# Optimization experiments

Measured on AMD Instinct MI355X. Metric: run time of the kernel, lower is better.

Reference implementation:

```python
import jax, jax.numpy as jnp
import numpy as np

B, S, H = 1, 1024, 1024
E = 1024          # expert_dim
NEXP = 16         # num_experts
TOPK = 2
ALPHA = 1.702
LIMIT = 7.0


def setup_inputs() -> dict:
    key = jax.random.key(0)
    ks = jax.random.split(key, 8)
    hidden_states = jax.random.normal(ks[0], (B, S, H), dtype=jnp.float32)
    # router (gate): Linear(H, NEXP) with bias
    Wg = jax.random.normal(ks[1], (NEXP, H), dtype=jnp.float32) / np.sqrt(H)
    bg = jax.random.normal(ks[2], (NEXP,), dtype=jnp.float32) * 0.01
    # per-expert gate_up_proj: Linear(H, 2E) -> store as [NEXP, H, 2E]
    Wgu = jax.random.normal(ks[3], (NEXP, H, 2 * E), dtype=jnp.float32) / np.sqrt(H)
    bgu = jax.random.normal(ks[4], (NEXP, 2 * E), dtype=jnp.float32) * 0.01
    # per-expert down_proj: Linear(E, H) -> store as [NEXP, E, H]
    Wd = jax.random.normal(ks[5], (NEXP, E, H), dtype=jnp.float32) / np.sqrt(E)
    bd = jax.random.normal(ks[6], (NEXP, H), dtype=jnp.float32) * 0.01
    return {"hidden_states": hidden_states, "Wg": Wg, "bg": bg,
            "Wgu": Wgu, "bgu": bgu, "Wd": Wd, "bd": bd}


def _moe_forward(x, Wg, bg, Wgu, bgu, Wd, bd):
    b, s, h = x.shape
    xt = x.reshape(-1, h)                                   # [T, H]
    # router
    logits = xt @ Wg.T + bg                                 # [T, NEXP]
    # gpt_oss routing: topk over raw logits, softmax over selected
    top_vals, top_idx = jax.lax.top_k(logits, TOPK)         # [T, K]
    rw = jax.nn.softmax(top_vals.astype(jnp.float32), axis=-1).astype(xt.dtype)
    # combine weight per (token, expert): zero for unselected experts
    onehot = jax.nn.one_hot(top_idx, NEXP, dtype=xt.dtype)  # [T, K, NEXP]
    cw = jnp.einsum("tk,tke->te", rw, onehot)               # [T, NEXP]
    # dense expert compute (reference math identical to gather/scatter version)
    gu = jnp.einsum("th,ehf->tef", xt, Wgu) + bgu[None]     # [T, NEXP, 2E]
    gate = gu[..., ::2]
    up = gu[..., 1::2]
    gate = jnp.minimum(gate, LIMIT)
    up = jnp.clip(up, -LIMIT, LIMIT)
    glu = gate * jax.nn.sigmoid(gate * ALPHA)
    gated = (up + 1.0) * glu                                # [T, NEXP, E]
    out_e = jnp.einsum("tef,efh->teh", gated, Wd) + bd[None]  # [T, NEXP, H]
    out = jnp.einsum("teh,te->th", out_e, cw)               # [T, H]
    return out.reshape(b, s, h)


def reference(hidden_states, Wg, bg, Wgu, bgu, Wd, bd):
    return _moe_forward(hidden_states, Wg, bg, Wgu, bgu, Wd, bd)
```

## Files before the change

### kernel.cpp

```cpp
#include <hip/hip_runtime.h>
#include <hip/hip_bf16.h>

#define NT 1024
#define HD 1024
#define ED 1024
#define F2D 2048
#define NEXPERT 16
#define GROWS 2304
#define ALPHA_C 1.702f
#define LIMIT_C 7.0f

typedef float f32x4 __attribute__((ext_vector_type(4)));
typedef short short8 __attribute__((ext_vector_type(8)));

__device__ __forceinline__ unsigned short f2bf(float x) {
  union { float f; unsigned int u; } v; v.f = x;
  unsigned int r = v.u + 0x7FFFu + ((v.u >> 16) & 1u);
  return (unsigned short)(r >> 16);
}
__device__ __forceinline__ unsigned int pk2(float lo, float hi) {
  return (unsigned int)f2bf(lo) | ((unsigned int)f2bf(hi) << 16);
}
__device__ __forceinline__ void async16(const void* g, void* l) {
  __builtin_amdgcn_global_load_lds((const __attribute__((address_space(1))) void*)g,
                                   (__attribute__((address_space(3))) void*)l, 16, 0, 0);
}

__global__ __launch_bounds__(64) void k_router(const float* __restrict__ x,
                                               const float* __restrict__ Wg,
                                               const float* __restrict__ bg,
                                               int* __restrict__ cnt,
                                               int* __restrict__ e01,
                                               float* __restrict__ w0f,
                                               float* __restrict__ w1f,
                                               unsigned short* __restrict__ Xbf) {
  const int t = blockIdx.x;
  const int l = threadIdx.x;
  const float4* x4 = (const float4*)(x + (size_t)t * HD);
  for (int i = 0; i < 4; ++i) {
    const int idx = l + 64 * i;
    float4 v = x4[idx];
    unsigned int a = pk2(v.x, v.y);
    unsigned int b = pk2(v.z, v.w);
    unsigned int* dst = (unsigned int*)(Xbf + (size_t)t * HD + idx * 4);
    dst[0] = a; dst[1] = b;
  }
  const int e = l & 15, qq = l >> 4;
  const float4* wg4 = (const float4*)(Wg + (size_t)e * HD);
  float s = 0.f;
  for (int j = 0; j < 64; ++j) {
    const int idx = qq + 4 * j;
    float4 a = x4[idx], b = wg4[idx];
    s += a.x * b.x + a.y * b.y + a.z * b.z + a.w * b.w;
  }
  s += __shfl_xor(s, 16);
  s += __shfl_xor(s, 32);
  const float logit = s + bg[e];
  float v0 = -1e30f, v1 = -1e30f; int i0 = 0, i1 = 0;
  for (int k = 0; k < 16; ++k) {
    float lv = __shfl(logit, k);
    if (lv > v0) { v1 = v0; i1 = i0; v0 = lv; i0 = k; }
    else if (lv > v1) { v1 = lv; i1 = k; }
  }
  if (l == 0) {
    float w0 = 1.f / (1.f + __expf(v1 - v0));
    atomicAdd(&cnt[i0], 1);
    atomicAdd(&cnt[i1], 1);
    e01[t] = i0 | (i1 << 8);
    w0f[t] = w0;
    w1f[t] = 1.f - w0;
  }
}

__global__ __launch_bounds__(1024) void k_scan_place(const int* __restrict__ cnt,
                                                     int* __restrict__ off,
                                                     const int* __restrict__ e01,
                                                     const float* __restrict__ w0f,
                                                     const float* __restrict__ w1f,
                                                     int* __restrict__ gtok,
                                                     float* __restrict__ gwt) {
  __shared__ int soff[NEXPERT];
  __shared__ int scur[NEXPERT];
  const int t = threadIdx.x;
  if (t == 0) {
    int a = 0;
    for (int e = 0; e < NEXPERT; ++e) { soff[e] = a; off[e] = a; a += cnt[e]; }
  }
  if (t < NEXPERT) scur[t] = 0;
  __syncthreads();
  const int p = e01[t];
  const int e0 = p & 255, e1 = p >> 8;
  int s0 = atomicAdd(&scur[e0], 1);
  int g0 = soff[e0] + s0;
  gtok[g0] = t; gwt[g0] = w0f[t];
  int s1 = atomicAdd(&scur[e1], 1);
  int g1 = soff[e1] + s1;
  gtok[g1] = t; gwt[g1] = w1f[t];
}

__global__ __launch_bounds__(256) void k_outinit(const float* __restrict__ bd,
                                                 const int* __restrict__ e01,
                                                 const float* __restrict__ w0f,
                                                 const float* __restrict__ w1f,
                                                 float* __restrict__ out) {
  const int t = blockIdx.x;
  const int h4 = threadIdx.x;
  const int p = e01[t];
  const int e0 = p & 255, e1 = p >> 8;
  const float w0 = w0f[t], w1 = w1f[t];
  float4 a = ((const float4*)(bd + (size_t)e0 * HD))[h4];
  float4 b = ((const float4*)(bd + (size_t)e1 * HD))[h4];
  float4 r;
  r.x = w0 * a.x + w1 * b.x;
  r.y = w0 * a.y + w1 * b.y;
  r.z = w0 * a.z + w1 * b.z;
  r.w = w0 * a.w + w1 * b.w;
  ((float4*)(out + (size_t)t * HD))[h4] = r;
}

__global__ __launch_bounds__(256) void k_gemm1(const unsigned short* __restrict__ Xbf,
                                               const float* __restrict__ Wgu,
                                               const float* __restrict__ bgu,
                                               const int* __restrict__ cnt,
                                               const int* __restrict__ off,
                                               const int* __restrict__ gtok,
                                               unsigned short* __restrict__ Gact) {
  const int e = blockIdx.z;
  const int Ne = cnt[e];
  const int mtile = blockIdx.y;
  if (mtile * 128 >= Ne) return;
  const int ntile = blockIdx.x;
  const int tid = threadIdx.x;
  const int lane = tid & 63;
  const int w = tid >> 6;
  const int wm = w & 1, wn = w >> 1;
  const int q = lane >> 4;
  const int fr = lane & 15;

  __shared__ unsigned short Alds[128 * 32];
  __shared__ unsigned int Blds[128 * 17];

  const int base = off[e] + mtile * 128;
  const int r0 = w * 32 + (lane >> 2);
  const int r1 = r0 + 16;
  const int c4 = lane & 3;
  const int gs0 = base + (((mtile * 128 + r0) < Ne) ? r0 : 0);
  const int gs1 = base + (((mtile * 128 + r1) < Ne) ? r1 : 0);
  const unsigned short* gp0 = Xbf + (size_t)gtok[gs0] * HD + c4 * 8;
  const unsigned short* gp1 = Xbf + (size_t)gtok[gs1] * HD + c4 * 8;
  unsigned short* la0 = Alds + w * 1024;
  unsigned short* la1 = Alds + w * 1024 + 512;
  const int k2 = tid >> 4;
  const int n8 = (tid & 15) * 8;
  const float* Wb = Wgu + (size_t)e * HD * F2D + (size_t)(2 * k2) * F2D + ntile * 128 + n8;

  f32x4 acc[4][4] = {};

  for (int ks = 0; ks < 32; ++ks) {
    __syncthreads();
    async16(gp0 + ks * 32, la0);
    async16(gp1 + ks * 32, la1);
    const float* bp = Wb + (size_t)ks * 32 * F2D;
    float4 a0 = *(const float4*)bp;
    float4 a1 = *(const float4*)(bp + 4);
    float4 b0 = *(const float4*)(bp + F2D);
    float4 b1 = *(const float4*)(bp + F2D + 4);
    Blds[(n8 + 0) * 17 + k2] = pk2(a0.x, b0.x);
    Blds[(n8 + 1) * 17 + k2] = pk2(a0.y, b0.y);
    Blds[(n8 + 2) * 17 + k2] = pk2(a0.z, b0.z);
    Blds[(n8 + 3) * 17 + k2] = pk2(a0.w, b0.w);
    Blds[(n8 + 4) * 17 + k2] = pk2(a1.x, b1.x);
    Blds[(n8 + 5) * 17 + k2] = pk2(a1.y, b1.y);
    Blds[(n8 + 6) * 17 + k2] = pk2(a1.z, b1.z);
    Blds[(n8 + 7) * 17 + k2] = pk2(a1.w, b1.w);
    __syncthreads();
    short8 af[4], bfr[4];
#pragma unroll
    for (int ni = 0; ni < 4; ++ni) {
      const unsigned int* p = Blds + (wn * 64 + ni * 16 + fr) * 17 + q * 4;
      union { unsigned int u[4]; short8 s; } uu;
      uu.u[0] = p[0]; uu.u[1] = p[1]; uu.u[2] = p[2]; uu.u[3] = p[3];
      bfr[ni] = uu.s;
    }
#pragma unroll
    for (int mi = 0; mi < 4; ++mi)
      af[mi] = *(const short8*)(Alds + (wm * 64 + mi * 16 + fr) * 32 + q * 8);
#pragma unroll
    for (int mi = 0; mi < 4; ++mi)
#pragma unroll
      for (int ni = 0; ni < 4; ++ni)
        acc[mi][ni] = __builtin_amdgcn_mfma_f32_16x16x32_bf16(af[mi], bfr[ni], acc[mi][ni], 0, 0, 0);
  }

  const float* bguE = bgu + (size_t)e * F2D + ntile * 128;
#pragma unroll
  for (int mi = 0; mi < 4; ++mi) {
    const int rowb = wm * 64 + mi * 16 + q * 4;
#pragma unroll
    for (int ni = 0; ni < 4; ++ni) {
      const int col = wn * 64 + ni * 16 + fr;
      const float bias = bguE[col];
#pragma unroll
      for (int r = 0; r < 4; ++r) {
        float v = acc[mi][ni][r] + bias;
        float pv = __shfl_xor(v, 1);
        float gate = (lane & 1) ? pv : v;
        float up   = (lane & 1) ? v : pv;
        gate = fminf(gate, LIMIT_C);
        up = fminf(fmaxf(up, -LIMIT_C), LIMIT_C);
        float glu = gate / (1.f + __expf(-ALPHA_C * gate));
        float val = (up + 1.f) * glu;
        const int s = rowb + r;
        if (!(lane & 1) && (mtile * 128 + s) < Ne)
          Gact[(size_t)(base + s) * ED + ntile * 64 + (col >> 1)] = f2bf(val);
      }
    }
  }
}

__global__ __launch_bounds__(256) void k_gemm2(const unsigned short* __restrict__ Gact,
                                               const float* __restrict__ Wd,
                                               const int* __restrict__ cnt,
                                               const int* __restrict__ off,
                                               const int* __restrict__ gtok,
                                               const float* __restrict__ gwt,
                                               float* __restrict__ out) {
  const int e = blockIdx.z;
  const int Ne = cnt[e];
  const int mtile = blockIdx.y;
  if (mtile * 128 >= Ne) return;
  const int ntile = blockIdx.x;
  const int tid = threadIdx.x;
  const int lane = tid & 63;
  const int w = tid >> 6;
  const int wm = w & 1, wn = w >> 1;
  const int q = lane >> 4;
  const int fr = lane & 15;

  __shared__ unsigned short Alds[128 * 32];
  __shared__ unsigned int Blds[128 * 17];

  const int base = off[e] + mtile * 128;
  const int r0 = w * 32 + (lane >> 2);
  const int r1 = r0 + 16;
  const int c4 = lane & 3;
  const unsigned short* gp0 = Gact + (size_t)(base + r0) * ED + c4 * 8;
  const unsigned short* gp1 = Gact + (size_t)(base + r1) * ED + c4 * 8;
  unsigned short* la0 = Alds + w * 1024;
  unsigned short* la1 = Alds + w * 1024 + 512;
  const int k2 = tid >> 4;
  const int n8 = (tid & 15) * 8;
  const float* Wb = Wd + (size_t)e * ED * HD + (size_t)(2 * k2) * HD + ntile * 128 + n8;

  f32x4 acc[4][4] = {};

  for (int ks = 0; ks < 32; ++ks) {
    __syncthreads();
    async16(gp0 + ks * 32, la0);
    async16(gp1 + ks * 32, la1);
    const float* bp = Wb + (size_t)ks * 32 * HD;
    float4 a0 = *(const float4*)bp;
    float4 a1 = *(const float4*)(bp + 4);
    float4 b0 = *(const float4*)(bp + HD);
    float4 b1 = *(const float4*)(bp + HD + 4);
    Blds[(n8 + 0) * 17 + k2] = pk2(a0.x, b0.x);
    Blds[(n8 + 1) * 17 + k2] = pk2(a0.y, b0.y);
    Blds[(n8 + 2) * 17 + k2] = pk2(a0.z, b0.z);
    Blds[(n8 + 3) * 17 + k2] = pk2(a0.w, b0.w);
    Blds[(n8 + 4) * 17 + k2] = pk2(a1.x, b1.x);
    Blds[(n8 + 5) * 17 + k2] = pk2(a1.y, b1.y);
    Blds[(n8 + 6) * 17 + k2] = pk2(a1.z, b1.z);
    Blds[(n8 + 7) * 17 + k2] = pk2(a1.w, b1.w);
    __syncthreads();
    short8 af[4], bfr[4];
#pragma unroll
    for (int ni = 0; ni < 4; ++ni) {
      const unsigned int* p = Blds + (wn * 64 + ni * 16 + fr) * 17 + q * 4;
      union { unsigned int u[4]; short8 s; } uu;
      uu.u[0] = p[0]; uu.u[1] = p[1]; uu.u[2] = p[2]; uu.u[3] = p[3];
      bfr[ni] = uu.s;
    }
#pragma unroll
    for (int mi = 0; mi < 4; ++mi)
      af[mi] = *(const short8*)(Alds + (wm * 64 + mi * 16 + fr) * 32 + q * 8);
#pragma unroll
    for (int mi = 0; mi < 4; ++mi)
#pragma unroll
      for (int ni = 0; ni < 4; ++ni)
        acc[mi][ni] = __builtin_amdgcn_mfma_f32_16x16x32_bf16(af[mi], bfr[ni], acc[mi][ni], 0, 0, 0);
  }

#pragma unroll
  for (int mi = 0; mi < 4; ++mi) {
    const int rowb = wm * 64 + mi * 16 + q * 4;
#pragma unroll
    for (int r = 0; r < 4; ++r) {
      const int s = rowb + r;
      if ((mtile * 128 + s) < Ne) {
        const int gsl = base + s;
        const int tok = gtok[gsl];
        const float wt = gwt[gsl];
        float* op = out + (size_t)tok * HD + ntile * 128;
#pragma unroll
        for (int ni = 0; ni < 4; ++ni) {
          const int col = wn * 64 + ni * 16 + fr;
          atomicAdd(op + col, wt * acc[mi][ni][r]);
        }
      }
    }
  }
}

extern "C" void kernel_launch(void* const* d_in, const int* in_sizes, int n_in,
                              void* d_out, int out_size, void* d_ws, size_t ws_size,
                              hipStream_t stream) {
  const float* x   = (const float*)d_in[0];
  const float* Wg  = (const float*)d_in[1];
  const float* bg  = (const float*)d_in[2];
  const float* Wgu = (const float*)d_in[3];
  const float* bgu = (const float*)d_in[4];
  const float* Wd  = (const float*)d_in[5];
  const float* bd  = (const float*)d_in[6];
  float* out = (float*)d_out;

  int* cnt = (int*)d_ws;
  int* off = cnt + 16;
  int* e01 = off + 16;
  float* w0f = (float*)(e01 + NT);
  float* w1f = w0f + NT;
  int* gtok = (int*)(w1f + NT);
  float* gwt = (float*)(gtok + GROWS);
  unsigned short* Xbf = (unsigned short*)(gwt + GROWS);
  unsigned short* Gact = Xbf + (size_t)NT * HD;

  hipMemsetAsync(cnt, 0, 16 * sizeof(int), stream);
  k_router<<<NT, 64, 0, stream>>>(x, Wg, bg, cnt, e01, w0f, w1f, Xbf);
  k_scan_place<<<1, NT, 0, stream>>>(cnt, off, e01, w0f, w1f, gtok, gwt);
  k_gemm1<<<dim3(16, 8, NEXPERT), 256, 0, stream>>>(Xbf, Wgu, bgu, cnt, off, gtok, Gact);
  k_outinit<<<NT, 256, 0, stream>>>(bd, e01, w0f, w1f, out);
  k_gemm2<<<dim3(8, 8, NEXPERT), 256, 0, stream>>>(Gact, Wd, cnt, off, gtok, gwt, out);
}
```

Measured before the change: 370.2 us.

## Double-buffer MoE GEMMs, shrink N tiles, split-K down proj, fuse routing kernels

Both expert GEMMs now double-buffer their LDS tiles. The next K-slice's weight loads and async activation copies are issued before the current slice's MFMAs, which removes one barrier per iteration. N tiles shrink from 128 to 64 columns and gemm2 adds a 2-way split-K, giving more blocks to fill the GPU on a memory-bound fp32 weight stream, plus a transposed B layout written with vector stores. The bias/output init moves into the router, and expert counting moves into the scan kernel, which drops a memset and a launch. The cost is more atomic adds to the output from split-K and smaller per-block reuse of the activation tiles.

```diff
diff --git a/kernel.cpp b/kernel.cpp
--- a/kernel.cpp
+++ b/kernel.cpp
@@ -12,6 +12,7 @@
 
 typedef float f32x4 __attribute__((ext_vector_type(4)));
 typedef short short8 __attribute__((ext_vector_type(8)));
+typedef unsigned int u32x4 __attribute__((ext_vector_type(4)));
 
 __device__ __forceinline__ unsigned short f2bf(float x) {
   union { float f; unsigned int u; } v; v.f = x;
@@ -29,11 +30,12 @@
 __global__ __launch_bounds__(64) void k_router(const float* __restrict__ x,
                                                const float* __restrict__ Wg,
                                                const float* __restrict__ bg,
-                                               int* __restrict__ cnt,
+                                               const float* __restrict__ bd,
                                                int* __restrict__ e01,
                                                float* __restrict__ w0f,
                                                float* __restrict__ w1f,
-                                               unsigned short* __restrict__ Xbf) {
+                                               unsigned short* __restrict__ Xbf,
+                                               float* __restrict__ out) {
   const int t = blockIdx.x;
   const int l = threadIdx.x;
   const float4* x4 = (const float4*)(x + (size_t)t * HD);
@@ -62,34 +64,51 @@
     if (lv > v0) { v1 = v0; i1 = i0; v0 = lv; i0 = k; }
     else if (lv > v1) { v1 = lv; i1 = k; }
   }
+  const float w0 = 1.f / (1.f + __expf(v1 - v0));
+  const float w1 = 1.f - w0;
   if (l == 0) {
-    float w0 = 1.f / (1.f + __expf(v1 - v0));
-    atomicAdd(&cnt[i0], 1);
-    atomicAdd(&cnt[i1], 1);
     e01[t] = i0 | (i1 << 8);
     w0f[t] = w0;
-    w1f[t] = 1.f - w0;
-  }
-}
-
-__global__ __launch_bounds__(1024) void k_scan_place(const int* __restrict__ cnt,
-                                                     int* __restrict__ off,
-                                                     const int* __restrict__ e01,
-                                                     const float* __restrict__ w0f,
-                                                     const float* __restrict__ w1f,
-                                                     int* __restrict__ gtok,
-                                                     float* __restrict__ gwt) {
+    w1f[t] = w1;
+  }
+  const float4* bd0 = (const float4*)(bd + (size_t)i0 * HD);
+  const float4* bd1 = (const float4*)(bd + (size_t)i1 * HD);
+  float4* o4 = (float4*)(out + (size_t)t * HD);
+  for (int i = 0; i < 4; ++i) {
+    const int idx = l + 64 * i;
+    float4 a = bd0[idx], b = bd1[idx];
+    float4 r;
+    r.x = w0 * a.x + w1 * b.x;
+    r.y = w0 * a.y + w1 * b.y;
+    r.z = w0 * a.z + w1 * b.z;
+    r.w = w0 * a.w + w1 * b.w;
+    o4[idx] = r;
+  }
+}
+
+__global__ __launch_bounds__(1024) void k_scan(const int* __restrict__ e01,
+                                               const float* __restrict__ w0f,
+                                               const float* __restrict__ w1f,
+                                               int* __restrict__ cnt,
+                                               int* __restrict__ off,
+                                               int* __restrict__ gtok,
+                                               float* __restrict__ gwt) {
+  __shared__ int scnt[NEXPERT];
   __shared__ int soff[NEXPERT];
   __shared__ int scur[NEXPERT];
   const int t = threadIdx.x;
+  if (t < NEXPERT) { scnt[t] = 0; scur[t] = 0; }
+  __syncthreads();
+  const int p = e01[t];
+  const int e0 = p & 255, e1 = p >> 8;
+  atomicAdd(&scnt[e0], 1);
+  atomicAdd(&scnt[e1], 1);
+  __syncthreads();
   if (t == 0) {
     int a = 0;
-    for (int e = 0; e < NEXPERT; ++e) { soff[e] = a; off[e] = a; a += cnt[e]; }
-  }
-  if (t < NEXPERT) scur[t] = 0;
-  __syncthreads();
-  const int p = e01[t];
-  const int e0 = p & 255, e1 = p >> 8;
+    for (int e = 0; e < NEXPERT; ++e) { soff[e] = a; off[e] = a; cnt[e] = scnt[e]; a += scnt[e]; }
+  }
+  __syncthreads();
   int s0 = atomicAdd(&scur[e0], 1);
   int g0 = soff[e0] + s0;
   gtok[g0] = t; gwt[g0] = w0f[t];
@@ -98,33 +117,13 @@
   gtok[g1] = t; gwt[g1] = w1f[t];
 }
 
-__global__ __launch_bounds__(256) void k_outinit(const float* __restrict__ bd,
-                                                 const int* __restrict__ e01,
-                                                 const float* __restrict__ w0f,
-                                                 const float* __restrict__ w1f,
-                                                 float* __restrict__ out) {
-  const int t = blockIdx.x;
-  const int h4 = threadIdx.x;
-  const int p = e01[t];
-  const int e0 = p & 255, e1 = p >> 8;
-  const float w0 = w0f[t], w1 = w1f[t];
-  float4 a = ((const float4*)(bd + (size_t)e0 * HD))[h4];
-  float4 b = ((const float4*)(bd + (size_t)e1 * HD))[h4];
-  float4 r;
-  r.x = w0 * a.x + w1 * b.x;
-  r.y = w0 * a.y + w1 * b.y;
-  r.z = w0 * a.z + w1 * b.z;
-  r.w = w0 * a.w + w1 * b.w;
-  ((float4*)(out + (size_t)t * HD))[h4] = r;
-}
-
-__global__ __launch_bounds__(256) void k_gemm1(const unsigned short* __restrict__ Xbf,
-                                               const float* __restrict__ Wgu,
-                                               const float* __restrict__ bgu,
-                                               const int* __restrict__ cnt,
-                                               const int* __restrict__ off,
-                                               const int* __restrict__ gtok,
-                                               unsigned short* __restrict__ Gact) {
+__global__ __launch_bounds__(256, 4) void k_gemm1(const unsigned short* __restrict__ Xbf,
+                                                  const float* __restrict__ Wgu,
+                                                  const float* __restrict__ bgu,
+                                                  const int* __restrict__ cnt,
+                                                  const int* __restrict__ off,
+                                                  const int* __restrict__ gtok,
+                                                  unsigned short* __restrict__ Gact) {
   const int e = blockIdx.z;
   const int Ne = cnt[e];
   const int mtile = blockIdx.y;
@@ -137,68 +136,81 @@
   const int q = lane >> 4;
   const int fr = lane & 15;
 
-  __shared__ unsigned short Alds[128 * 32];
-  __shared__ unsigned int Blds[128 * 17];
+  __shared__ unsigned short Alds[2 * 128 * 32];
+  __shared__ unsigned int Blds[2 * 16 * 68];
 
   const int base = off[e] + mtile * 128;
   const int r0 = w * 32 + (lane >> 2);
   const int r1 = r0 + 16;
-  const int c4 = lane & 3;
+  const int c4a = lane & 3;
   const int gs0 = base + (((mtile * 128 + r0) < Ne) ? r0 : 0);
   const int gs1 = base + (((mtile * 128 + r1) < Ne) ? r1 : 0);
-  const unsigned short* gp0 = Xbf + (size_t)gtok[gs0] * HD + c4 * 8;
-  const unsigned short* gp1 = Xbf + (size_t)gtok[gs1] * HD + c4 * 8;
-  unsigned short* la0 = Alds + w * 1024;
-  unsigned short* la1 = Alds + w * 1024 + 512;
+  const unsigned short* gp0 = Xbf + (size_t)gtok[gs0] * HD + c4a * 8;
+  const unsigned short* gp1 = Xbf + (size_t)gtok[gs1] * HD + c4a * 8;
+  const int lofs = w * 1024;
+
   const int k2 = tid >> 4;
-  const int n8 = (tid & 15) * 8;
-  const float* Wb = Wgu + (size_t)e * HD * F2D + (size_t)(2 * k2) * F2D + ntile * 128 + n8;
-
-  f32x4 acc[4][4] = {};
-
+  const int c4 = tid & 15;
+  const float* Wb = Wgu + (size_t)e * HD * F2D + (size_t)(2 * k2) * F2D + ntile * 64 + c4 * 4;
+
+  f32x4 acc[4][2] = {};
+  float4 ba, bb;
+
+  ba = *(const float4*)Wb;
+  bb = *(const float4*)(Wb + F2D);
+  async16(gp0, Alds + lofs);
+  async16(gp1, Alds + lofs + 512);
+  {
+    u32x4 pkv;
+    pkv[0] = pk2(ba.x, bb.x); pkv[1] = pk2(ba.y, bb.y);
+    pkv[2] = pk2(ba.z, bb.z); pkv[3] = pk2(ba.w, bb.w);
+    *(u32x4*)(Blds + k2 * 68 + c4 * 4) = pkv;
+  }
+  __syncthreads();
+
+#pragma unroll 2
   for (int ks = 0; ks < 32; ++ks) {
+    const int cur = ks & 1, nxt = cur ^ 1;
+    const bool more = (ks + 1) < 32;
+    if (more) {
+      const float* bp = Wb + (size_t)(ks + 1) * 32 * F2D;
+      ba = *(const float4*)bp;
+      bb = *(const float4*)(bp + F2D);
+      async16(gp0 + (ks + 1) * 32, Alds + nxt * 4096 + lofs);
+      async16(gp1 + (ks + 1) * 32, Alds + nxt * 4096 + lofs + 512);
+    }
+    short8 af[4], bfr[2];
+#pragma unroll
+    for (int mi = 0; mi < 4; ++mi)
+      af[mi] = *(const short8*)(Alds + cur * 4096 + (wm * 64 + mi * 16 + fr) * 32 + q * 8);
+#pragma unroll
+    for (int ni = 0; ni < 2; ++ni) {
+      const unsigned int* p = Blds + cur * 1088 + q * 4 * 68 + wn * 32 + ni * 16 + fr;
+      union { unsigned int u[4]; short8 s; } uu;
+      uu.u[0] = p[0]; uu.u[1] = p[68]; uu.u[2] = p[136]; uu.u[3] = p[204];
+      bfr[ni] = uu.s;
+    }
+#pragma unroll
+    for (int mi = 0; mi < 4; ++mi)
+#pragma unroll
+      for (int ni = 0; ni < 2; ++ni)
+        acc[mi][ni] = __builtin_amdgcn_mfma_f32_16x16x32_bf16(af[mi], bfr[ni], acc[mi][ni], 0, 0, 0);
+    if (more) {
+      u32x4 pkv;
+      pkv[0] = pk2(ba.x, bb.x); pkv[1] = pk2(ba.y, bb.y);
+      pkv[2] = pk2(ba.z, bb.z); pkv[3] = pk2(ba.w, bb.w);
+      *(u32x4*)(Blds + nxt * 1088 + k2 * 68 + c4 * 4) = pkv;
+    }
     __syncthreads();
-    async16(gp0 + ks * 32, la0);
-    async16(gp1 + ks * 32, la1);
-    const float* bp = Wb + (size_t)ks * 32 * F2D;
-    float4 a0 = *(const float4*)bp;
-    float4 a1 = *(const float4*)(bp + 4);
-    float4 b0 = *(const float4*)(bp + F2D);
-    float4 b1 = *(const float4*)(bp + F2D + 4);
-    Blds[(n8 + 0) * 17 + k2] = pk2(a0.x, b0.x);
-    Blds[(n8 + 1) * 17 + k2] = pk2(a0.y, b0.y);
-    Blds[(n8 + 2) * 17 + k2] = pk2(a0.z, b0.z);
-    Blds[(n8 + 3) * 17 + k2] = pk2(a0.w, b0.w);
-    Blds[(n8 + 4) * 17 + k2] = pk2(a1.x, b1.x);
-    Blds[(n8 + 5) * 17 + k2] = pk2(a1.y, b1.y);
-    Blds[(n8 + 6) * 17 + k2] = pk2(a1.z, b1.z);
-    Blds[(n8 + 7) * 17 + k2] = pk2(a1.w, b1.w);
-    __syncthreads();
-    short8 af[4], bfr[4];
-#pragma unroll
-    for (int ni = 0; ni < 4; ++ni) {
-      const unsigned int* p = Blds + (wn * 64 + ni * 16 + fr) * 17 + q * 4;
-      union { unsigned int u[4]; short8 s; } uu;
-      uu.u[0] = p[0]; uu.u[1] = p[1]; uu.u[2] = p[2]; uu.u[3] = p[3];
-      bfr[ni] = uu.s;
-    }
-#pragma unroll
-    for (int mi = 0; mi < 4; ++mi)
-      af[mi] = *(const short8*)(Alds + (wm * 64 + mi * 16 + fr) * 32 + q * 8);
-#pragma unroll
-    for (int mi = 0; mi < 4; ++mi)
-#pragma unroll
-      for (int ni = 0; ni < 4; ++ni)
-        acc[mi][ni] = __builtin_amdgcn_mfma_f32_16x16x32_bf16(af[mi], bfr[ni], acc[mi][ni], 0, 0, 0);
-  }
-
-  const float* bguE = bgu + (size_t)e * F2D + ntile * 128;
+  }
+
+  const float* bguE = bgu + (size_t)e * F2D + ntile * 64;
 #pragma unroll
   for (int mi = 0; mi < 4; ++mi) {
     const int rowb = wm * 64 + mi * 16 + q * 4;
 #pragma unroll
-    for (int ni = 0; ni < 4; ++ni) {
-      const int col = wn * 64 + ni * 16 + fr;
+    for (int ni = 0; ni < 2; ++ni) {
+      const int col = wn * 32 + ni * 16 + fr;
       const float bias = bguE[col];
 #pragma unroll
       for (int r = 0; r < 4; ++r) {
@@ -212,20 +224,21 @@
         float val = (up + 1.f) * glu;
         const int s = rowb + r;
         if (!(lane & 1) && (mtile * 128 + s) < Ne)
-          Gact[(size_t)(base + s) * ED + ntile * 64 + (col >> 1)] = f2bf(val);
+          Gact[(size_t)(base + s) * ED + ntile * 32 + (col >> 1)] = f2bf(val);
       }
     }
   }
 }
 
-__global__ __launch_bounds__(256) void k_gemm2(const unsigned short* __restrict__ Gact,
-                                               const float* __restrict__ Wd,
-                                               const int* __restrict__ cnt,
-                                               const int* __restrict__ off,
-                                               const int* __restrict__ gtok,
-                                               const float* __restrict__ gwt,
-                                               float* __restrict__ out) {
-  const int e = blockIdx.z;
+__global__ __launch_bounds__(256, 4) void k_gemm2(const unsigned short* __restrict__ Gact,
+                                                  const float* __restrict__ Wd,
+                                                  const int* __restrict__ cnt,
+                                                  const int* __restrict__ off,
+                                                  const int* __restrict__ gtok,
+                                                  const float* __restrict__ gwt,
+                                                  float* __restrict__ out) {
+  const int z = blockIdx.z;
+  const int e = z >> 1, ksp = z & 1;
   const int Ne = cnt[e];
   const int mtile = blockIdx.y;
   if (mtile * 128 >= Ne) return;
@@ -237,57 +250,70 @@
   const int q = lane >> 4;
   const int fr = lane & 15;
 
-  __shared__ unsigned short Alds[128 * 32];
-  __shared__ unsigned int Blds[128 * 17];
+  __shared__ unsigned short Alds[2 * 128 * 32];
+  __shared__ unsigned int Blds[2 * 16 * 68];
 
   const int base = off[e] + mtile * 128;
   const int r0 = w * 32 + (lane >> 2);
   const int r1 = r0 + 16;
-  const int c4 = lane & 3;
-  const unsigned short* gp0 = Gact + (size_t)(base + r0) * ED + c4 * 8;
-  const unsigned short* gp1 = Gact + (size_t)(base + r1) * ED + c4 * 8;
-  unsigned short* la0 = Alds + w * 1024;
-  unsigned short* la1 = Alds + w * 1024 + 512;
+  const int c4a = lane & 3;
+  const unsigned short* gp0 = Gact + (size_t)(base + r0) * ED + ksp * 512 + c4a * 8;
+  const unsigned short* gp1 = Gact + (size_t)(base + r1) * ED + ksp * 512 + c4a * 8;
+  const int lofs = w * 1024;
+
   const int k2 = tid >> 4;
-  const int n8 = (tid & 15) * 8;
-  const float* Wb = Wd + (size_t)e * ED * HD + (size_t)(2 * k2) * HD + ntile * 128 + n8;
-
-  f32x4 acc[4][4] = {};
-
-  for (int ks = 0; ks < 32; ++ks) {
+  const int c4 = tid & 15;
+  const float* Wb = Wd + (size_t)e * ED * HD + (size_t)(ksp * 512 + 2 * k2) * HD + ntile * 64 + c4 * 4;
+
+  f32x4 acc[4][2] = {};
+  float4 ba, bb;
+
+  ba = *(const float4*)Wb;
+  bb = *(const float4*)(Wb + HD);
+  async16(gp0, Alds + lofs);
+  async16(gp1, Alds + lofs + 512);
+  {
+    u32x4 pkv;
+    pkv[0] = pk2(ba.x, bb.x); pkv[1] = pk2(ba.y, bb.y);
+    pkv[2] = pk2(ba.z, bb.z); pkv[3] = pk2(ba.w, bb.w);
+    *(u32x4*)(Blds + k2 * 68 + c4 * 4) = pkv;
+  }
+  __syncthreads();
+
+#pragma unroll 2
+  for (int ks = 0; ks < 16; ++ks) {
+    const int cur = ks & 1, nxt = cur ^ 1;
+    const bool more = (ks + 1) < 16;
+    if (more) {
+      const float* bp = Wb + (size_t)(ks + 1) * 32 * HD;
+      ba = *(const float4*)bp;
+      bb = *(const float4*)(bp + HD);
+      async16(gp0 + (ks + 1) * 32, Alds + nxt * 4096 + lofs);
+      async16(gp1 + (ks + 1) * 32, Alds + nxt * 4096 + lofs + 512);
+    }
+    short8 af[4], bfr[2];
+#pragma unroll
+    for (int mi = 0; mi < 4; ++mi)
+      af[mi] = *(const short8*)(Alds + cur * 4096 + (wm * 64 + mi * 16 + fr) * 32 + q * 8);
+#pragma unroll
+    for (int ni = 0; ni < 2; ++ni) {
+      const unsigned int* p = Blds + cur * 1088 + q * 4 * 68 + wn * 32 + ni * 16 + fr;
+      union { unsigned int u[4]; short8 s; } uu;
+      uu.u[0] = p[0]; uu.u[1] = p[68]; uu.u[2] = p[136]; uu.u[3] = p[204];
+      bfr[ni] = uu.s;
+    }
+#pragma unroll
+    for (int mi = 0; mi < 4; ++mi)
+#pragma unroll
+      for (int ni = 0; ni < 2; ++ni)
+        acc[mi][ni] = __builtin_amdgcn_mfma_f32_16x16x32_bf16(af[mi], bfr[ni], acc[mi][ni], 0, 0, 0);
+    if (more) {
+      u32x4 pkv;
+      pkv[0] = pk2(ba.x, bb.x); pkv[1] = pk2(ba.y, bb.y);
+      pkv[2] = pk2(ba.z, bb.z); pkv[3] = pk2(ba.w, bb.w);
+      *(u32x4*)(Blds + nxt * 1088 + k2 * 68 + c4 * 4) = pkv;
+    }
     __syncthreads();
-    async16(gp0 + ks * 32, la0);
-    async16(gp1 + ks * 32, la1);
-    const float* bp = Wb + (size_t)ks * 32 * HD;
-    float4 a0 = *(const float4*)bp;
-    float4 a1 = *(const float4*)(bp + 4);
-    float4 b0 = *(const float4*)(bp + HD);
-    float4 b1 = *(const float4*)(bp + HD + 4);
-    Blds[(n8 + 0) * 17 + k2] = pk2(a0.x, b0.x);
-    Blds[(n8 + 1) * 17 + k2] = pk2(a0.y, b0.y);
-    Blds[(n8 + 2) * 17 + k2] = pk2(a0.z, b0.z);
-    Blds[(n8 + 3) * 17 + k2] = pk2(a0.w, b0.w);
-    Blds[(n8 + 4) * 17 + k2] = pk2(a1.x, b1.x);
-    Blds[(n8 + 5) * 17 + k2] = pk2(a1.y, b1.y);
-    Blds[(n8 + 6) * 17 + k2] = pk2(a1.z, b1.z);
-    Blds[(n8 + 7) * 17 + k2] = pk2(a1.w, b1.w);
-    __syncthreads();
-    short8 af[4], bfr[4];
-#pragma unroll
-    for (int ni = 0; ni < 4; ++ni) {
-      const unsigned int* p = Blds + (wn * 64 + ni * 16 + fr) * 17 + q * 4;
-      union { unsigned int u[4]; short8 s; } uu;
-      uu.u[0] = p[0]; uu.u[1] = p[1]; uu.u[2] = p[2]; uu.u[3] = p[3];
-      bfr[ni] = uu.s;
-    }
-#pragma unroll
-    for (int mi = 0; mi < 4; ++mi)
-      af[mi] = *(const short8*)(Alds + (wm * 64 + mi * 16 + fr) * 32 + q * 8);
-#pragma unroll
-    for (int mi = 0; mi < 4; ++mi)
-#pragma unroll
-      for (int ni = 0; ni < 4; ++ni)
-        acc[mi][ni] = __builtin_amdgcn_mfma_f32_16x16x32_bf16(af[mi], bfr[ni], acc[mi][ni], 0, 0, 0);
   }
 
 #pragma unroll
@@ -300,10 +326,10 @@
         const int gsl = base + s;
         const int tok = gtok[gsl];
         const float wt = gwt[gsl];
-        float* op = out + (size_t)tok * HD + ntile * 128;
-#pragma unroll
-        for (int ni = 0; ni < 4; ++ni) {
-          const int col = wn * 64 + ni * 16 + fr;
+        float* op = out + (size_t)tok * HD + ntile * 64;
+#pragma unroll
+        for (int ni = 0; ni < 2; ++ni) {
+          const int col = wn * 32 + ni * 16 + fr;
           atomicAdd(op + col, wt * acc[mi][ni][r]);
         }
       }
@@ -333,10 +359,8 @@
   unsigned short* Xbf = (unsigned short*)(gwt + GROWS);
   unsigned short* Gact = Xbf + (size_t)NT * HD;
 
-  hipMemsetAsync(cnt, 0, 16 * sizeof(int), stream);
-  k_router<<<NT, 64, 0, stream>>>(x, Wg, bg, cnt, e01, w0f, w1f, Xbf);
-  k_scan_place<<<1, NT, 0, stream>>>(cnt, off, e01, w0f, w1f, gtok, gwt);
-  k_gemm1<<<dim3(16, 8, NEXPERT), 256, 0, stream>>>(Xbf, Wgu, bgu, cnt, off, gtok, Gact);
-  k_outinit<<<NT, 256, 0, stream>>>(bd, e01, w0f, w1f, out);
-  k_gemm2<<<dim3(8, 8, NEXPERT), 256, 0, stream>>>(Gact, Wd, cnt, off, gtok, gwt, out);
-}
+  k_router<<<NT, 64, 0, stream>>>(x, Wg, bg, bd, e01, w0f, w1f, Xbf, out);
+  k_scan<<<1, NT, 0, stream>>>(e01, w0f, w1f, cnt, off, gtok, gwt);
+  k_gemm1<<<dim3(32, 8, NEXPERT), 256, 0, stream>>>(Xbf, Wgu, bgu, cnt, off, gtok, Gact);
+  k_gemm2<<<dim3(16, 8, 2 * NEXPERT), 256, 0, stream>>>(Gact, Wd, cnt, off, gtok, gwt, out);
+}
```

New measurement: 345.9 us. 6.6% less time.
